# Optimization experiments

Measured on AMD Instinct MI355X. Metric: run time of the kernel, lower is better.

The kernel has to match this reference:

```python
import jax, jax.numpy as jnp
import numpy as np

EPS = 1e-8
N, IN_F, H, NRBF = 1024, 64, 32, 50
CUT_UP = 5.0  # cutoff_upper; cutoff_lower = 0 -> alpha = 5/(5-0) = 1


def setup_inputs() -> dict:
    key = jax.random.key(0)
    ks = jax.random.split(key, 6)
    start = float(np.exp(-CUT_UP))  # exp(-cutoff_upper + cutoff_lower)
    means = jnp.linspace(start, 1.0, NRBF).astype(jnp.float32)
    betas = jnp.full((NRBF,), (2.0 / NRBF * (1.0 - start)) ** (-2), dtype=jnp.float32)
    return {
        "h": jax.random.normal(ks[0], (N, IN_F), jnp.float32),
        "x": jax.random.normal(ks[1], (N, 3), jnp.float32),
        "W_fc": jax.random.normal(ks[2], (IN_F, H), jnp.float32) / np.float32(np.sqrt(IN_F)),
        "W_edge": jax.random.normal(ks[3], (NRBF, H), jnp.float32) / np.float32(np.sqrt(NRBF)),
        "means": means,
        "betas": betas,
        "W1": jax.random.normal(ks[4], (H, H), jnp.float32) / np.float32(np.sqrt(H)),
        "b1": jnp.zeros((H,), jnp.float32),
        "W2": jax.random.normal(ks[5], (H, 1), jnp.float32) / np.float32(np.sqrt(H)),
        "b2": jnp.zeros((1,), jnp.float32),
    }


def reference(h, x, W_fc, W_edge, means, betas, W1, b1, W2, b2):
    hp = h @ W_fc                                      # (N, H)
    delta = x[None, :, :] - x[:, None, :]              # (N, N, 3) pairwise deltas
    s = (delta ** 2).sum(-1, keepdims=True)            # (N, N, 1) squared distance
    dist = jax.nn.relu(s) + EPS                        # note: squared distance, as in source
    delta_n = delta / jnp.sqrt(jax.nn.relu(s + EPS))   # (N, N, 3)
    # ExpNormalSmearing: cosine_cutoff(dist) * exp(-betas*(exp(-dist) - means)^2)
    cut = 0.5 * (jnp.cos(jnp.pi * (2.0 * dist / CUT_UP + 1.0)) + 1.0)
    rbf = cut * jnp.exp(-betas * (jnp.exp(-dist) - means) ** 2)  # (N, N, NRBF)
    he = rbf @ W_edge                                  # (N, N, H)
    h_e_vec = he[..., :, None] * delta_n[..., None, :] # (N, N, H, 3)
    ese = hp[:, None, :] + hp[None, :, :]              # (N, N, H)
    comb = ese[..., None] * h_e_vec                    # (N, N, H, 3)
    cnorm = (comb ** 2).sum(-1)                        # (N, N, H)
    e = jax.nn.sigmoid(cnorm @ W1 + b1) @ W2 + b2      # (N, N, 1)
    return e.sum(axis=(-2, -3))                        # (1,)
```

## Files before the change

kernel.cpp:

```cpp
#include <hip/hip_runtime.h>
#include <hip/hip_bf16.h>
#include <math.h>

#define N_ATOMS 1024
#define IN_F 64
#define H_DIM 32
#define NRBF 50
#define TILE 16
#define NT 64
#define NBT 2080
#define TBL 4096
#define SASTR 40

typedef short bf16x8 __attribute__((ext_vector_type(8)));
typedef float f32x4  __attribute__((ext_vector_type(4)));

static __device__ __forceinline__ unsigned short f2bf(float f) {
    unsigned int u = __float_as_uint(f);
    u += 0x7fffu + ((u >> 16) & 1u);
    return (unsigned short)(u >> 16);
}

__global__ __launch_bounds__(256) void prep_kernel(
    const float* __restrict__ h, const float* __restrict__ W_fc,
    const float* __restrict__ W_edge, const float* __restrict__ means,
    const float* __restrict__ betas, const float* __restrict__ W1,
    const float* __restrict__ b1, const float* __restrict__ W2,
    float* __restrict__ hp, unsigned short* __restrict__ Gb,
    unsigned short* __restrict__ Wp, float2* __restrict__ bw,
    int* __restrict__ tt)
{
    const int blk = blockIdx.x;
    const int t = threadIdx.x;
    if (blk < 128) {
        int id = blk * 256 + t;
        int i = id >> 5, o = id & 31;
        float acc = 0.f;
        #pragma unroll 8
        for (int k = 0; k < IN_F; ++k)
            acc += h[i * IN_F + k] * W_fc[k * H_DIM + o];
        hp[i * H_DIM + o] = acc;
    } else if (blk < 192) {
        int id = (blk - 128) * 256 + t;
        int idx = id >> 2, c0 = (id & 3) * 8;
        float ed = (float)idx * (1.0f / (float)(TBL - 1));
        float acc[8];
        #pragma unroll
        for (int c = 0; c < 8; ++c) acc[c] = 0.f;
        for (int k = 0; k < NRBF; ++k) {
            float d = ed - means[k];
            float wv = __expf(-betas[k] * d * d);
            #pragma unroll
            for (int c = 0; c < 8; ++c)
                acc[c] += wv * W_edge[k * H_DIM + c0 + c];
        }
        bf16x8 pk;
        #pragma unroll
        for (int c = 0; c < 8; ++c) pk[c] = (short)f2bf(acc[c]);
        *(bf16x8*)&Gb[idx * H_DIM + c0] = pk;
    } else if (blk < 201) {
        int e = (blk - 192) * 256 + t;
        if (e < NBT) {
            int ti = (int)(64.5f - sqrtf(64.5f * 64.5f - 2.0f * (float)e));
            ti = ti < 0 ? 0 : (ti > NT - 1 ? NT - 1 : ti);
            while ((ti + 1) * NT - ((ti + 1) * ti) / 2 <= e) ++ti;
            while (ti > 0 && ti * NT - (ti * (ti - 1)) / 2 > e) --ti;
            int tj = ti + (e - (ti * NT - (ti * (ti - 1)) / 2));
            tt[e] = (ti << 8) | tj;
        }
    } else {
        #pragma unroll
        for (int q = 0; q < 4; ++q) {
            int f  = t * 4 + q;
            int ct = f >> 9, ln = (f >> 3) & 63, j = f & 7;
            int c0f = ln & 15, kb = (ln >> 4) * 8;
            Wp[f] = f2bf(W1[(kb + j) * H_DIM + c0f + 16 * ct]);
        }
        if (t < 32) { float2 v; v.x = b1[t]; v.y = W2[t]; bw[t] = v; }
    }
}

__global__ __launch_bounds__(256, 6) void pair_kernel(
    const float* __restrict__ x, const float* __restrict__ hp,
    const unsigned short* __restrict__ Gb, const unsigned short* __restrict__ Wp,
    const float2* __restrict__ bw, const int* __restrict__ tt,
    float* __restrict__ partials)
{
    __shared__ float shpi[TILE][36], shpj[TILE][36];
    __shared__ unsigned short sA[256 * SASTR];
    __shared__ float swave[4];

    const int t    = threadIdx.x;
    const int lane = t & 63;
    const int w    = t >> 6;
    const int c0f  = lane & 15;
    const int b    = blockIdx.x;

    const int tv = tt[b];
    const int ti = tv >> 8, tj = tv & 255;
    const int i0 = ti * TILE, j0 = tj * TILE;
    const float wgt = (ti == tj) ? 1.0f : 2.0f;

    const int li = t >> 4;
    const int lj = t & 15;

    const float xi0 = x[(i0 + li) * 3 + 0];
    const float xi1 = x[(i0 + li) * 3 + 1];
    const float xi2 = x[(i0 + li) * 3 + 2];
    const float xj0 = x[(j0 + lj) * 3 + 0];
    const float xj1 = x[(j0 + lj) * 3 + 1];
    const float xj2 = x[(j0 + lj) * 3 + 2];

    if (t < 128) {
        int r = t >> 3, c = t & 7;
        *(float4*)&shpi[r][c * 4] = *(const float4*)&hp[(i0 + r) * H_DIM + c * 4];
    } else {
        int u = t - 128, r = u >> 3, c = u & 7;
        *(float4*)&shpj[r][c * 4] = *(const float4*)&hp[(j0 + r) * H_DIM + c * 4];
    }

    bf16x8 bfrag0 = *(const bf16x8*)&Wp[lane * 8];
    bf16x8 bfrag1 = *(const bf16x8*)&Wp[512 + lane * 8];
    const float2 bw0 = bw[c0f];
    const float2 bw1 = bw[c0f + 16];

    const float dx = xj0 - xi0, dy = xj1 - xi1, dz = xj2 - xi2;
    const float s  = dx * dx + dy * dy + dz * dz;
    const float dist = s + 1e-8f;
    const float dn2  = s / (s + 1e-8f);
    const float sn   = __sinf(0.62831853f * dist);
    const float K    = dn2 * (sn * sn) * (sn * sn);
    const float ed   = __expf(-dist);

    float uu = ed * (float)(TBL - 1);
    int idx  = (int)(uu + 0.5f);
    if (idx > TBL - 1) idx = TBL - 1;
    const unsigned short* __restrict__ r0 = Gb + idx * H_DIM;
    const bf16x8 gA = *(const bf16x8*)(r0);
    const bf16x8 gB = *(const bf16x8*)(r0 + 8);
    const bf16x8 gC = *(const bf16x8*)(r0 + 16);
    const bf16x8 gD = *(const bf16x8*)(r0 + 24);

    __syncthreads();

    const int sw = (t >> 3) & 3;
    #pragma unroll
    for (int q = 0; q < 4; ++q) {
        const bf16x8 gs = (q == 0) ? gA : (q == 1) ? gB : (q == 2) ? gC : gD;
        union { bf16x8 v8; unsigned int u[4]; } gu, pk;
        gu.v8 = gs;
        const float4 hi0 = *(const float4*)&shpi[li][q * 8];
        const float4 hi1 = *(const float4*)&shpi[li][q * 8 + 4];
        const float4 hj0 = *(const float4*)&shpj[lj][q * 8];
        const float4 hj1 = *(const float4*)&shpj[lj][q * 8 + 4];
        float e0 = hi0.x + hj0.x, e1 = hi0.y + hj0.y;
        float e2 = hi0.z + hj0.z, e3 = hi0.w + hj0.w;
        float e4 = hi1.x + hj1.x, e5 = hi1.y + hj1.y;
        float e6 = hi1.z + hj1.z, e7 = hi1.w + hj1.w;
        float g0 = __uint_as_float(gu.u[0] << 16);
        float g1 = __uint_as_float(gu.u[0] & 0xffff0000u);
        float g2 = __uint_as_float(gu.u[1] << 16);
        float g3 = __uint_as_float(gu.u[1] & 0xffff0000u);
        float g4 = __uint_as_float(gu.u[2] << 16);
        float g5 = __uint_as_float(gu.u[2] & 0xffff0000u);
        float g6 = __uint_as_float(gu.u[3] << 16);
        float g7 = __uint_as_float(gu.u[3] & 0xffff0000u);
        float v0 = e0 * g0, v1 = e1 * g1, v2 = e2 * g2, v3 = e3 * g3;
        float v4 = e4 * g4, v5 = e5 * g5, v6 = e6 * g6, v7 = e7 * g7;
        float c0 = v0 * v0 * K, c1 = v1 * v1 * K, c2 = v2 * v2 * K, c3 = v3 * v3 * K;
        float c4 = v4 * v4 * K, c5 = v5 * v5 * K, c6 = v6 * v6 * K, c7 = v7 * v7 * K;
        pk.u[0] = ((__float_as_uint(c0) + 0x8000u) >> 16) | ((__float_as_uint(c1) + 0x8000u) & 0xffff0000u);
        pk.u[1] = ((__float_as_uint(c2) + 0x8000u) >> 16) | ((__float_as_uint(c3) + 0x8000u) & 0xffff0000u);
        pk.u[2] = ((__float_as_uint(c4) + 0x8000u) >> 16) | ((__float_as_uint(c5) + 0x8000u) & 0xffff0000u);
        pk.u[3] = ((__float_as_uint(c6) + 0x8000u) >> 16) | ((__float_as_uint(c7) + 0x8000u) & 0xffff0000u);
        *(bf16x8*)&sA[t * SASTR + (q ^ sw) * 8] = pk.v8;
    }
    __syncthreads();

    float p = 0.f;
    #pragma unroll
    for (int rt = 0; rt < 4; ++rt) {
        const int row = w * 64 + rt * 16 + c0f;
        const int rq  = (lane >> 4) ^ ((row >> 3) & 3);
        bf16x8 afrag = *(const bf16x8*)&sA[row * SASTR + rq * 8];
        f32x4 acc0 = {0.f, 0.f, 0.f, 0.f};
        acc0 = __builtin_amdgcn_mfma_f32_16x16x32_bf16(afrag, bfrag0, acc0, 0, 0, 0);
        f32x4 acc1 = {0.f, 0.f, 0.f, 0.f};
        acc1 = __builtin_amdgcn_mfma_f32_16x16x32_bf16(afrag, bfrag1, acc1, 0, 0, 0);
        #pragma unroll
        for (int r = 0; r < 4; ++r) {
            const float av0 = acc0[r] + bw0.x;
            p += bw0.y * __builtin_amdgcn_rcpf(1.0f + __expf(-av0));
            const float av1 = acc1[r] + bw1.x;
            p += bw1.y * __builtin_amdgcn_rcpf(1.0f + __expf(-av1));
        }
    }

    float v = wgt * p;
    #pragma unroll
    for (int off = 32; off > 0; off >>= 1)
        v += __shfl_down(v, off);
    if (lane == 0) swave[w] = v;
    __syncthreads();
    if (t == 0)
        partials[b] = (swave[0] + swave[1]) + (swave[2] + swave[3]);
}

__global__ __launch_bounds__(256) void reduce_kernel(
    const float* __restrict__ partials, const float* __restrict__ b2,
    float* __restrict__ out)
{
    __shared__ float sm[256];
    const int t = threadIdx.x;
    float a = 0.f;
    for (int u = t; u < NBT; u += 256) a += partials[u];
    sm[t] = a;
    __syncthreads();
    for (int off = 128; off > 0; off >>= 1) {
        if (t < off) sm[t] += sm[t + off];
        __syncthreads();
    }
    if (t == 0)
        out[0] = sm[0] + (float)N_ATOMS * (float)N_ATOMS * b2[0];
}

extern "C" void kernel_launch(void* const* d_in, const int* in_sizes, int n_in,
                              void* d_out, int out_size, void* d_ws, size_t ws_size,
                              hipStream_t stream) {
    const float* h      = (const float*)d_in[0];
    const float* x      = (const float*)d_in[1];
    const float* W_fc   = (const float*)d_in[2];
    const float* W_edge = (const float*)d_in[3];
    const float* means  = (const float*)d_in[4];
    const float* betas  = (const float*)d_in[5];
    const float* W1     = (const float*)d_in[6];
    const float* b1     = (const float*)d_in[7];
    const float* W2     = (const float*)d_in[8];
    const float* b2     = (const float*)d_in[9];
    float* out = (float*)d_out;

    char* base = (char*)d_ws;
    float*          ws_partials = (float*)base;
    float*          ws_hp       = (float*)(base + 10240);
    unsigned short* ws_Gb       = (unsigned short*)(base + 141312);
    unsigned short* ws_Wp       = (unsigned short*)(base + 403456);
    float2*         ws_bw       = (float2*)(base + 405504);
    int*            ws_tt       = (int*)(base + 405760);

    prep_kernel<<<202, 256, 0, stream>>>(h, W_fc, W_edge, means, betas,
                                         W1, b1, W2, ws_hp, ws_Gb, ws_Wp,
                                         ws_bw, ws_tt);
    pair_kernel<<<NBT, 256, 0, stream>>>(x, ws_hp, ws_Gb, ws_Wp, ws_bw,
                                         ws_tt, ws_partials);
    reduce_kernel<<<1, 256, 0, stream>>>(ws_partials, b2, out);
}
```

Before: 24.22 us.

## Build MFMA A-fragments directly in registers, dropping LDS staging and syncs

Each lane now computes the pair features for exactly the MFMA A-fragment slot it owns (row i, column j, k-slice), so the LDS staging buffer, the hp tiles in shared memory and two barriers go away. The RBF lookup table is stored as fp32 instead of bf16, so each lane fetches two float4s for its k-slice. The pair geometry (distance, sine, exp) is now recomputed by every k-slice lane, four times more often than before, and hp and x are read straight from global or cache. Occupancy is raised to 8 blocks per SM through the launch bounds.

```diff
diff --git a/kernel.cpp b/kernel.cpp
--- a/kernel.cpp
+++ b/kernel.cpp
@@ -10,7 +10,6 @@
 #define NT 64
 #define NBT 2080
 #define TBL 4096
-#define SASTR 40
 
 typedef short bf16x8 __attribute__((ext_vector_type(8)));
 typedef float f32x4  __attribute__((ext_vector_type(4)));
@@ -26,7 +25,7 @@
     const float* __restrict__ W_edge, const float* __restrict__ means,
     const float* __restrict__ betas, const float* __restrict__ W1,
     const float* __restrict__ b1, const float* __restrict__ W2,
-    float* __restrict__ hp, unsigned short* __restrict__ Gb,
+    float* __restrict__ hp, float* __restrict__ Gf,
     unsigned short* __restrict__ Wp, float2* __restrict__ bw,
     int* __restrict__ tt)
 {
@@ -54,10 +53,8 @@
             for (int c = 0; c < 8; ++c)
                 acc[c] += wv * W_edge[k * H_DIM + c0 + c];
         }
-        bf16x8 pk;
-        #pragma unroll
-        for (int c = 0; c < 8; ++c) pk[c] = (short)f2bf(acc[c]);
-        *(bf16x8*)&Gb[idx * H_DIM + c0] = pk;
+        #pragma unroll
+        for (int c = 0; c < 8; ++c) Gf[idx * H_DIM + c0 + c] = acc[c];
     } else if (blk < 201) {
         int e = (blk - 192) * 256 + t;
         if (e < NBT) {
@@ -80,20 +77,19 @@
     }
 }
 
-__global__ __launch_bounds__(256, 6) void pair_kernel(
+__global__ __launch_bounds__(256, 8) void pair_kernel(
     const float* __restrict__ x, const float* __restrict__ hp,
-    const unsigned short* __restrict__ Gb, const unsigned short* __restrict__ Wp,
+    const float* __restrict__ Gf, const unsigned short* __restrict__ Wp,
     const float2* __restrict__ bw, const int* __restrict__ tt,
     float* __restrict__ partials)
 {
-    __shared__ float shpi[TILE][36], shpj[TILE][36];
-    __shared__ unsigned short sA[256 * SASTR];
     __shared__ float swave[4];
 
     const int t    = threadIdx.x;
     const int lane = t & 63;
     const int w    = t >> 6;
     const int c0f  = lane & 15;
+    const int kb   = (lane >> 4) * 8;
     const int b    = blockIdx.x;
 
     const int tv = tt[b];
@@ -101,92 +97,69 @@
     const int i0 = ti * TILE, j0 = tj * TILE;
     const float wgt = (ti == tj) ? 1.0f : 2.0f;
 
-    const int li = t >> 4;
-    const int lj = t & 15;
-
-    const float xi0 = x[(i0 + li) * 3 + 0];
-    const float xi1 = x[(i0 + li) * 3 + 1];
-    const float xi2 = x[(i0 + li) * 3 + 2];
-    const float xj0 = x[(j0 + lj) * 3 + 0];
-    const float xj1 = x[(j0 + lj) * 3 + 1];
-    const float xj2 = x[(j0 + lj) * 3 + 2];
-
-    if (t < 128) {
-        int r = t >> 3, c = t & 7;
-        *(float4*)&shpi[r][c * 4] = *(const float4*)&hp[(i0 + r) * H_DIM + c * 4];
-    } else {
-        int u = t - 128, r = u >> 3, c = u & 7;
-        *(float4*)&shpj[r][c * 4] = *(const float4*)&hp[(j0 + r) * H_DIM + c * 4];
-    }
-
-    bf16x8 bfrag0 = *(const bf16x8*)&Wp[lane * 8];
-    bf16x8 bfrag1 = *(const bf16x8*)&Wp[512 + lane * 8];
+    const float4 hja = *(const float4*)&hp[(j0 + c0f) * H_DIM + kb];
+    const float4 hjb = *(const float4*)&hp[(j0 + c0f) * H_DIM + kb + 4];
+    const float xj0 = x[(j0 + c0f) * 3 + 0];
+    const float xj1 = x[(j0 + c0f) * 3 + 1];
+    const float xj2 = x[(j0 + c0f) * 3 + 2];
+
+    const bf16x8 bfrag0 = *(const bf16x8*)&Wp[lane * 8];
+    const bf16x8 bfrag1 = *(const bf16x8*)&Wp[512 + lane * 8];
     const float2 bw0 = bw[c0f];
     const float2 bw1 = bw[c0f + 16];
 
-    const float dx = xj0 - xi0, dy = xj1 - xi1, dz = xj2 - xi2;
-    const float s  = dx * dx + dy * dy + dz * dz;
-    const float dist = s + 1e-8f;
-    const float dn2  = s / (s + 1e-8f);
-    const float sn   = __sinf(0.62831853f * dist);
-    const float K    = dn2 * (sn * sn) * (sn * sn);
-    const float ed   = __expf(-dist);
-
-    float uu = ed * (float)(TBL - 1);
-    int idx  = (int)(uu + 0.5f);
-    if (idx > TBL - 1) idx = TBL - 1;
-    const unsigned short* __restrict__ r0 = Gb + idx * H_DIM;
-    const bf16x8 gA = *(const bf16x8*)(r0);
-    const bf16x8 gB = *(const bf16x8*)(r0 + 8);
-    const bf16x8 gC = *(const bf16x8*)(r0 + 16);
-    const bf16x8 gD = *(const bf16x8*)(r0 + 24);
-
-    __syncthreads();
-
-    const int sw = (t >> 3) & 3;
+    float p = 0.f;
+
     #pragma unroll
-    for (int q = 0; q < 4; ++q) {
-        const bf16x8 gs = (q == 0) ? gA : (q == 1) ? gB : (q == 2) ? gC : gD;
-        union { bf16x8 v8; unsigned int u[4]; } gu, pk;
-        gu.v8 = gs;
-        const float4 hi0 = *(const float4*)&shpi[li][q * 8];
-        const float4 hi1 = *(const float4*)&shpi[li][q * 8 + 4];
-        const float4 hj0 = *(const float4*)&shpj[lj][q * 8];
-        const float4 hj1 = *(const float4*)&shpj[lj][q * 8 + 4];
-        float e0 = hi0.x + hj0.x, e1 = hi0.y + hj0.y;
-        float e2 = hi0.z + hj0.z, e3 = hi0.w + hj0.w;
-        float e4 = hi1.x + hj1.x, e5 = hi1.y + hj1.y;
-        float e6 = hi1.z + hj1.z, e7 = hi1.w + hj1.w;
-        float g0 = __uint_as_float(gu.u[0] << 16);
-        float g1 = __uint_as_float(gu.u[0] & 0xffff0000u);
-        float g2 = __uint_as_float(gu.u[1] << 16);
-        float g3 = __uint_as_float(gu.u[1] & 0xffff0000u);
-        float g4 = __uint_as_float(gu.u[2] << 16);
-        float g5 = __uint_as_float(gu.u[2] & 0xffff0000u);
-        float g6 = __uint_as_float(gu.u[3] << 16);
-        float g7 = __uint_as_float(gu.u[3] & 0xffff0000u);
-        float v0 = e0 * g0, v1 = e1 * g1, v2 = e2 * g2, v3 = e3 * g3;
-        float v4 = e4 * g4, v5 = e5 * g5, v6 = e6 * g6, v7 = e7 * g7;
-        float c0 = v0 * v0 * K, c1 = v1 * v1 * K, c2 = v2 * v2 * K, c3 = v3 * v3 * K;
-        float c4 = v4 * v4 * K, c5 = v5 * v5 * K, c6 = v6 * v6 * K, c7 = v7 * v7 * K;
+    for (int rt = 0; rt < 4; ++rt) {
+        const int ri = w * 4 + rt;
+        const float xi0 = x[(i0 + ri) * 3 + 0];
+        const float xi1 = x[(i0 + ri) * 3 + 1];
+        const float xi2 = x[(i0 + ri) * 3 + 2];
+
+        const float dx = xj0 - xi0, dy = xj1 - xi1, dz = xj2 - xi2;
+        const float s  = dx * dx + dy * dy + dz * dz;
+        const float dist = s + 1e-8f;
+        const float dn2  = s / (s + 1e-8f);
+        const float sn   = __sinf(0.62831853f * dist);
+        const float K    = dn2 * (sn * sn) * (sn * sn);
+        const float ed   = __expf(-dist);
+
+        float uu = ed * (float)(TBL - 1);
+        int idx  = (int)(uu + 0.5f);
+        if (idx > TBL - 1) idx = TBL - 1;
+
+        const float* __restrict__ gp = Gf + idx * H_DIM + kb;
+        const float4 ga = *(const float4*)gp;
+        const float4 gb = *(const float4*)(gp + 4);
+
+        const float4 hia = *(const float4*)&hp[(i0 + ri) * H_DIM + kb];
+        const float4 hib = *(const float4*)&hp[(i0 + ri) * H_DIM + kb + 4];
+
+        const float v0 = (hia.x + hja.x) * ga.x;
+        const float v1 = (hia.y + hja.y) * ga.y;
+        const float v2 = (hia.z + hja.z) * ga.z;
+        const float v3 = (hia.w + hja.w) * ga.w;
+        const float v4 = (hib.x + hjb.x) * gb.x;
+        const float v5 = (hib.y + hjb.y) * gb.y;
+        const float v6 = (hib.z + hjb.z) * gb.z;
+        const float v7 = (hib.w + hjb.w) * gb.w;
+        const float c0 = v0 * v0 * K, c1 = v1 * v1 * K;
+        const float c2 = v2 * v2 * K, c3 = v3 * v3 * K;
+        const float c4 = v4 * v4 * K, c5 = v5 * v5 * K;
+        const float c6 = v6 * v6 * K, c7 = v7 * v7 * K;
+
+        union { bf16x8 v8; unsigned int u[4]; } pk;
         pk.u[0] = ((__float_as_uint(c0) + 0x8000u) >> 16) | ((__float_as_uint(c1) + 0x8000u) & 0xffff0000u);
         pk.u[1] = ((__float_as_uint(c2) + 0x8000u) >> 16) | ((__float_as_uint(c3) + 0x8000u) & 0xffff0000u);
         pk.u[2] = ((__float_as_uint(c4) + 0x8000u) >> 16) | ((__float_as_uint(c5) + 0x8000u) & 0xffff0000u);
         pk.u[3] = ((__float_as_uint(c6) + 0x8000u) >> 16) | ((__float_as_uint(c7) + 0x8000u) & 0xffff0000u);
-        *(bf16x8*)&sA[t * SASTR + (q ^ sw) * 8] = pk.v8;
-    }
-    __syncthreads();
-
-    float p = 0.f;
-    #pragma unroll
-    for (int rt = 0; rt < 4; ++rt) {
-        const int row = w * 64 + rt * 16 + c0f;
-        const int rq  = (lane >> 4) ^ ((row >> 3) & 3);
-        bf16x8 afrag = *(const bf16x8*)&sA[row * SASTR + rq * 8];
+
         f32x4 acc0 = {0.f, 0.f, 0.f, 0.f};
-        acc0 = __builtin_amdgcn_mfma_f32_16x16x32_bf16(afrag, bfrag0, acc0, 0, 0, 0);
+        acc0 = __builtin_amdgcn_mfma_f32_16x16x32_bf16(pk.v8, bfrag0, acc0, 0, 0, 0);
         f32x4 acc1 = {0.f, 0.f, 0.f, 0.f};
-        acc1 = __builtin_amdgcn_mfma_f32_16x16x32_bf16(afrag, bfrag1, acc1, 0, 0, 0);
+        acc1 = __builtin_amdgcn_mfma_f32_16x16x32_bf16(pk.v8, bfrag1, acc1, 0, 0, 0);
+
         #pragma unroll
         for (int r = 0; r < 4; ++r) {
             const float av0 = acc0[r] + bw0.x;
@@ -242,15 +215,15 @@
     char* base = (char*)d_ws;
     float*          ws_partials = (float*)base;
     float*          ws_hp       = (float*)(base + 10240);
-    unsigned short* ws_Gb       = (unsigned short*)(base + 141312);
-    unsigned short* ws_Wp       = (unsigned short*)(base + 403456);
-    float2*         ws_bw       = (float2*)(base + 405504);
-    int*            ws_tt       = (int*)(base + 405760);
+    float*          ws_Gf       = (float*)(base + 141312);
+    unsigned short* ws_Wp       = (unsigned short*)(base + 665600);
+    float2*         ws_bw       = (float2*)(base + 667648);
+    int*            ws_tt       = (int*)(base + 667904);
 
     prep_kernel<<<202, 256, 0, stream>>>(h, W_fc, W_edge, means, betas,
-                                         W1, b1, W2, ws_hp, ws_Gb, ws_Wp,
+                                         W1, b1, W2, ws_hp, ws_Gf, ws_Wp,
                                          ws_bw, ws_tt);
-    pair_kernel<<<NBT, 256, 0, stream>>>(x, ws_hp, ws_Gb, ws_Wp, ws_bw,
+    pair_kernel<<<NBT, 256, 0, stream>>>(x, ws_hp, ws_Gf, ws_Wp, ws_bw,
                                          ws_tt, ws_partials);
     reduce_kernel<<<1, 256, 0, stream>>>(ws_partials, b2, out);
 }
```

Result: slower. 34.50 us (+42.4%).

## Process two j-tiles per block to halve block count in pair kernel

Applied to the files above, without the earlier changes.

Each block now handles one 16-row i-tile against a 32-column j-strip split into two 16x16 sub-tiles, with the triangular tile enumeration remapped to row pairs. This halves the number of blocks and reuses the i-side positions and hp rows across both sub-tiles, cutting per-block setup and launch overhead. The lower-triangle sub-tile is skipped through a zero weight. The change adds an extra barrier, serialises the two sub-tiles within a block, raises register pressure, and lowers the occupancy hint from 6 to 5.

```diff
diff --git a/kernel.cpp b/kernel.cpp
--- a/kernel.cpp
+++ b/kernel.cpp
@@ -8,7 +8,7 @@
 #define NRBF 50
 #define TILE 16
 #define NT 64
-#define NBT 2080
+#define NBLK 1056
 #define TBL 4096
 #define SASTR 40
 
@@ -58,15 +58,18 @@
         #pragma unroll
         for (int c = 0; c < 8; ++c) pk[c] = (short)f2bf(acc[c]);
         *(bf16x8*)&Gb[idx * H_DIM + c0] = pk;
-    } else if (blk < 201) {
+    } else if (blk < 197) {
         int e = (blk - 192) * 256 + t;
-        if (e < NBT) {
-            int ti = (int)(64.5f - sqrtf(64.5f * 64.5f - 2.0f * (float)e));
-            ti = ti < 0 ? 0 : (ti > NT - 1 ? NT - 1 : ti);
-            while ((ti + 1) * NT - ((ti + 1) * ti) / 2 <= e) ++ti;
-            while (ti > 0 && ti * NT - (ti * (ti - 1)) / 2 > e) --ti;
-            int tj = ti + (e - (ti * NT - (ti * (ti - 1)) / 2));
-            tt[e] = (ti << 8) | tj;
+        if (e < NBLK) {
+            int a = (int)((65.0f - sqrtf(65.0f * 65.0f - 4.0f * (float)e)) * 0.5f);
+            a = a < 0 ? 0 : (a > 31 ? 31 : a);
+            while (a > 0 && a * (65 - a) > e) --a;
+            while ((a + 1) * (65 - (a + 1)) <= e) ++a;
+            int e1 = e - a * (65 - a);
+            int ti, tj2;
+            if (e1 < 32 - a) { ti = 2 * a;     tj2 = a + e1; }
+            else             { ti = 2 * a + 1; tj2 = a + e1 - (32 - a); }
+            tt[e] = (ti << 8) | tj2;
         }
     } else {
         #pragma unroll
@@ -80,13 +83,13 @@
     }
 }
 
-__global__ __launch_bounds__(256, 6) void pair_kernel(
+__global__ __launch_bounds__(256, 5) void pair_kernel(
     const float* __restrict__ x, const float* __restrict__ hp,
     const unsigned short* __restrict__ Gb, const unsigned short* __restrict__ Wp,
     const float2* __restrict__ bw, const int* __restrict__ tt,
     float* __restrict__ partials)
 {
-    __shared__ float shpi[TILE][36], shpj[TILE][36];
+    __shared__ float shpi[TILE][36], shpjA[TILE][36], shpjB[TILE][36];
     __shared__ unsigned short sA[256 * SASTR];
     __shared__ float swave[4];
 
@@ -96,10 +99,13 @@
     const int c0f  = lane & 15;
     const int b    = blockIdx.x;
 
-    const int tv = tt[b];
-    const int ti = tv >> 8, tj = tv & 255;
-    const int i0 = ti * TILE, j0 = tj * TILE;
-    const float wgt = (ti == tj) ? 1.0f : 2.0f;
+    const int tv  = tt[b];
+    const int ti  = tv >> 8, tj2 = tv & 255;
+    const int i0  = ti * TILE;
+    const int j0A = tj2 * 32, j0B = j0A + 16;
+    const int tjA = 2 * tj2, tjB = tjA + 1;
+    const float wgtA = (tjA < ti) ? 0.f : (tjA == ti ? 1.f : 2.f);
+    const float wgtB = (tjB == ti) ? 1.f : 2.f;
 
     const int li = t >> 4;
     const int lj = t & 15;
@@ -107,96 +113,168 @@
     const float xi0 = x[(i0 + li) * 3 + 0];
     const float xi1 = x[(i0 + li) * 3 + 1];
     const float xi2 = x[(i0 + li) * 3 + 2];
-    const float xj0 = x[(j0 + lj) * 3 + 0];
-    const float xj1 = x[(j0 + lj) * 3 + 1];
-    const float xj2 = x[(j0 + lj) * 3 + 2];
+    const float xA0 = x[(j0A + lj) * 3 + 0];
+    const float xA1 = x[(j0A + lj) * 3 + 1];
+    const float xA2 = x[(j0A + lj) * 3 + 2];
+    const float xB0 = x[(j0B + lj) * 3 + 0];
+    const float xB1 = x[(j0B + lj) * 3 + 1];
+    const float xB2 = x[(j0B + lj) * 3 + 2];
 
     if (t < 128) {
         int r = t >> 3, c = t & 7;
-        *(float4*)&shpi[r][c * 4] = *(const float4*)&hp[(i0 + r) * H_DIM + c * 4];
+        *(float4*)&shpi[r][c * 4]  = *(const float4*)&hp[(i0 + r) * H_DIM + c * 4];
+        *(float4*)&shpjB[r][c * 4] = *(const float4*)&hp[(j0B + r) * H_DIM + c * 4];
     } else {
         int u = t - 128, r = u >> 3, c = u & 7;
-        *(float4*)&shpj[r][c * 4] = *(const float4*)&hp[(j0 + r) * H_DIM + c * 4];
-    }
-
-    bf16x8 bfrag0 = *(const bf16x8*)&Wp[lane * 8];
-    bf16x8 bfrag1 = *(const bf16x8*)&Wp[512 + lane * 8];
+        *(float4*)&shpjA[r][c * 4] = *(const float4*)&hp[(j0A + r) * H_DIM + c * 4];
+    }
+
+    const bf16x8 bfrag0 = *(const bf16x8*)&Wp[lane * 8];
+    const bf16x8 bfrag1 = *(const bf16x8*)&Wp[512 + lane * 8];
     const float2 bw0 = bw[c0f];
     const float2 bw1 = bw[c0f + 16];
 
-    const float dx = xj0 - xi0, dy = xj1 - xi1, dz = xj2 - xi2;
-    const float s  = dx * dx + dy * dy + dz * dz;
-    const float dist = s + 1e-8f;
-    const float dn2  = s / (s + 1e-8f);
-    const float sn   = __sinf(0.62831853f * dist);
-    const float K    = dn2 * (sn * sn) * (sn * sn);
-    const float ed   = __expf(-dist);
-
-    float uu = ed * (float)(TBL - 1);
-    int idx  = (int)(uu + 0.5f);
-    if (idx > TBL - 1) idx = TBL - 1;
-    const unsigned short* __restrict__ r0 = Gb + idx * H_DIM;
-    const bf16x8 gA = *(const bf16x8*)(r0);
-    const bf16x8 gB = *(const bf16x8*)(r0 + 8);
-    const bf16x8 gC = *(const bf16x8*)(r0 + 16);
-    const bf16x8 gD = *(const bf16x8*)(r0 + 24);
+    float dx = xA0 - xi0, dy = xA1 - xi1, dz = xA2 - xi2;
+    float sA_ = dx * dx + dy * dy + dz * dz;
+    const float distA = sA_ + 1e-8f;
+    const float dn2A  = sA_ / (sA_ + 1e-8f);
+    const float snA   = __sinf(0.62831853f * distA);
+    const float KA    = dn2A * (snA * snA) * (snA * snA);
+    const float edA   = __expf(-distA);
+    float uuA = edA * (float)(TBL - 1);
+    int idxA  = (int)(uuA + 0.5f);
+    if (idxA > TBL - 1) idxA = TBL - 1;
+    const unsigned short* __restrict__ rA = Gb + idxA * H_DIM;
+    const bf16x8 gA0 = *(const bf16x8*)(rA);
+    const bf16x8 gA1 = *(const bf16x8*)(rA + 8);
+    const bf16x8 gA2 = *(const bf16x8*)(rA + 16);
+    const bf16x8 gA3 = *(const bf16x8*)(rA + 24);
+
+    dx = xB0 - xi0; dy = xB1 - xi1; dz = xB2 - xi2;
+    float sB_ = dx * dx + dy * dy + dz * dz;
+    const float distB = sB_ + 1e-8f;
+    const float dn2B  = sB_ / (sB_ + 1e-8f);
+    const float snB   = __sinf(0.62831853f * distB);
+    const float KB    = dn2B * (snB * snB) * (snB * snB);
+    const float edB   = __expf(-distB);
+    float uuB = edB * (float)(TBL - 1);
+    int idxB  = (int)(uuB + 0.5f);
+    if (idxB > TBL - 1) idxB = TBL - 1;
+    const unsigned short* __restrict__ rB = Gb + idxB * H_DIM;
+    const bf16x8 gB0 = *(const bf16x8*)(rB);
+    const bf16x8 gB1 = *(const bf16x8*)(rB + 8);
+    const bf16x8 gB2 = *(const bf16x8*)(rB + 16);
+    const bf16x8 gB3 = *(const bf16x8*)(rB + 24);
 
     __syncthreads();
 
     const int sw = (t >> 3) & 3;
-    #pragma unroll
-    for (int q = 0; q < 4; ++q) {
-        const bf16x8 gs = (q == 0) ? gA : (q == 1) ? gB : (q == 2) ? gC : gD;
-        union { bf16x8 v8; unsigned int u[4]; } gu, pk;
-        gu.v8 = gs;
-        const float4 hi0 = *(const float4*)&shpi[li][q * 8];
-        const float4 hi1 = *(const float4*)&shpi[li][q * 8 + 4];
-        const float4 hj0 = *(const float4*)&shpj[lj][q * 8];
-        const float4 hj1 = *(const float4*)&shpj[lj][q * 8 + 4];
-        float e0 = hi0.x + hj0.x, e1 = hi0.y + hj0.y;
-        float e2 = hi0.z + hj0.z, e3 = hi0.w + hj0.w;
-        float e4 = hi1.x + hj1.x, e5 = hi1.y + hj1.y;
-        float e6 = hi1.z + hj1.z, e7 = hi1.w + hj1.w;
-        float g0 = __uint_as_float(gu.u[0] << 16);
-        float g1 = __uint_as_float(gu.u[0] & 0xffff0000u);
-        float g2 = __uint_as_float(gu.u[1] << 16);
-        float g3 = __uint_as_float(gu.u[1] & 0xffff0000u);
-        float g4 = __uint_as_float(gu.u[2] << 16);
-        float g5 = __uint_as_float(gu.u[2] & 0xffff0000u);
-        float g6 = __uint_as_float(gu.u[3] << 16);
-        float g7 = __uint_as_float(gu.u[3] & 0xffff0000u);
-        float v0 = e0 * g0, v1 = e1 * g1, v2 = e2 * g2, v3 = e3 * g3;
-        float v4 = e4 * g4, v5 = e5 * g5, v6 = e6 * g6, v7 = e7 * g7;
-        float c0 = v0 * v0 * K, c1 = v1 * v1 * K, c2 = v2 * v2 * K, c3 = v3 * v3 * K;
-        float c4 = v4 * v4 * K, c5 = v5 * v5 * K, c6 = v6 * v6 * K, c7 = v7 * v7 * K;
-        pk.u[0] = ((__float_as_uint(c0) + 0x8000u) >> 16) | ((__float_as_uint(c1) + 0x8000u) & 0xffff0000u);
-        pk.u[1] = ((__float_as_uint(c2) + 0x8000u) >> 16) | ((__float_as_uint(c3) + 0x8000u) & 0xffff0000u);
-        pk.u[2] = ((__float_as_uint(c4) + 0x8000u) >> 16) | ((__float_as_uint(c5) + 0x8000u) & 0xffff0000u);
-        pk.u[3] = ((__float_as_uint(c6) + 0x8000u) >> 16) | ((__float_as_uint(c7) + 0x8000u) & 0xffff0000u);
-        *(bf16x8*)&sA[t * SASTR + (q ^ sw) * 8] = pk.v8;
-    }
-    __syncthreads();
-
     float p = 0.f;
-    #pragma unroll
-    for (int rt = 0; rt < 4; ++rt) {
-        const int row = w * 64 + rt * 16 + c0f;
-        const int rq  = (lane >> 4) ^ ((row >> 3) & 3);
-        bf16x8 afrag = *(const bf16x8*)&sA[row * SASTR + rq * 8];
-        f32x4 acc0 = {0.f, 0.f, 0.f, 0.f};
-        acc0 = __builtin_amdgcn_mfma_f32_16x16x32_bf16(afrag, bfrag0, acc0, 0, 0, 0);
-        f32x4 acc1 = {0.f, 0.f, 0.f, 0.f};
-        acc1 = __builtin_amdgcn_mfma_f32_16x16x32_bf16(afrag, bfrag1, acc1, 0, 0, 0);
-        #pragma unroll
-        for (int r = 0; r < 4; ++r) {
-            const float av0 = acc0[r] + bw0.x;
-            p += bw0.y * __builtin_amdgcn_rcpf(1.0f + __expf(-av0));
-            const float av1 = acc1[r] + bw1.x;
-            p += bw1.y * __builtin_amdgcn_rcpf(1.0f + __expf(-av1));
-        }
-    }
-
-    float v = wgt * p;
+
+    if (wgtA != 0.f) {
+        #pragma unroll
+        for (int q = 0; q < 4; ++q) {
+            const bf16x8 gs = (q == 0) ? gA0 : (q == 1) ? gA1 : (q == 2) ? gA2 : gA3;
+            union { bf16x8 v8; unsigned int u[4]; } gu, pk;
+            gu.v8 = gs;
+            const float4 hi0 = *(const float4*)&shpi[li][q * 8];
+            const float4 hi1 = *(const float4*)&shpi[li][q * 8 + 4];
+            const float4 hj0 = *(const float4*)&shpjA[lj][q * 8];
+            const float4 hj1 = *(const float4*)&shpjA[lj][q * 8 + 4];
+            float g0 = __uint_as_float(gu.u[0] << 16);
+            float g1 = __uint_as_float(gu.u[0] & 0xffff0000u);
+            float g2 = __uint_as_float(gu.u[1] << 16);
+            float g3 = __uint_as_float(gu.u[1] & 0xffff0000u);
+            float g4 = __uint_as_float(gu.u[2] << 16);
+            float g5 = __uint_as_float(gu.u[2] & 0xffff0000u);
+            float g6 = __uint_as_float(gu.u[3] << 16);
+            float g7 = __uint_as_float(gu.u[3] & 0xffff0000u);
+            float v0 = (hi0.x + hj0.x) * g0, v1 = (hi0.y + hj0.y) * g1;
+            float v2 = (hi0.z + hj0.z) * g2, v3 = (hi0.w + hj0.w) * g3;
+            float v4 = (hi1.x + hj1.x) * g4, v5 = (hi1.y + hj1.y) * g5;
+            float v6 = (hi1.z + hj1.z) * g6, v7 = (hi1.w + hj1.w) * g7;
+            float c0 = v0 * v0 * KA, c1 = v1 * v1 * KA, c2 = v2 * v2 * KA, c3 = v3 * v3 * KA;
+            float c4 = v4 * v4 * KA, c5 = v5 * v5 * KA, c6 = v6 * v6 * KA, c7 = v7 * v7 * KA;
+            pk.u[0] = ((__float_as_uint(c0) + 0x8000u) >> 16) | ((__float_as_uint(c1) + 0x8000u) & 0xffff0000u);
+            pk.u[1] = ((__float_as_uint(c2) + 0x8000u) >> 16) | ((__float_as_uint(c3) + 0x8000u) & 0xffff0000u);
+            pk.u[2] = ((__float_as_uint(c4) + 0x8000u) >> 16) | ((__float_as_uint(c5) + 0x8000u) & 0xffff0000u);
+            pk.u[3] = ((__float_as_uint(c6) + 0x8000u) >> 16) | ((__float_as_uint(c7) + 0x8000u) & 0xffff0000u);
+            *(bf16x8*)&sA[t * SASTR + (q ^ sw) * 8] = pk.v8;
+        }
+        __syncthreads();
+
+        float pA = 0.f;
+        #pragma unroll
+        for (int rt = 0; rt < 4; ++rt) {
+            const int row = w * 64 + rt * 16 + c0f;
+            const int rq  = (lane >> 4) ^ ((row >> 3) & 3);
+            bf16x8 afrag = *(const bf16x8*)&sA[row * SASTR + rq * 8];
+            f32x4 acc0 = {0.f, 0.f, 0.f, 0.f};
+            acc0 = __builtin_amdgcn_mfma_f32_16x16x32_bf16(afrag, bfrag0, acc0, 0, 0, 0);
+            f32x4 acc1 = {0.f, 0.f, 0.f, 0.f};
+            acc1 = __builtin_amdgcn_mfma_f32_16x16x32_bf16(afrag, bfrag1, acc1, 0, 0, 0);
+            #pragma unroll
+            for (int r = 0; r < 4; ++r) {
+                pA += bw0.y * __builtin_amdgcn_rcpf(1.0f + __expf(-(acc0[r] + bw0.x)));
+                pA += bw1.y * __builtin_amdgcn_rcpf(1.0f + __expf(-(acc1[r] + bw1.x)));
+            }
+        }
+        p += wgtA * pA;
+        __syncthreads();
+    }
+
+    {
+        #pragma unroll
+        for (int q = 0; q < 4; ++q) {
+            const bf16x8 gs = (q == 0) ? gB0 : (q == 1) ? gB1 : (q == 2) ? gB2 : gB3;
+            union { bf16x8 v8; unsigned int u[4]; } gu, pk;
+            gu.v8 = gs;
+            const float4 hi0 = *(const float4*)&shpi[li][q * 8];
+            const float4 hi1 = *(const float4*)&shpi[li][q * 8 + 4];
+            const float4 hj0 = *(const float4*)&shpjB[lj][q * 8];
+            const float4 hj1 = *(const float4*)&shpjB[lj][q * 8 + 4];
+            float g0 = __uint_as_float(gu.u[0] << 16);
+            float g1 = __uint_as_float(gu.u[0] & 0xffff0000u);
+            float g2 = __uint_as_float(gu.u[1] << 16);
+            float g3 = __uint_as_float(gu.u[1] & 0xffff0000u);
+            float g4 = __uint_as_float(gu.u[2] << 16);
+            float g5 = __uint_as_float(gu.u[2] & 0xffff0000u);
+            float g6 = __uint_as_float(gu.u[3] << 16);
+            float g7 = __uint_as_float(gu.u[3] & 0xffff0000u);
+            float v0 = (hi0.x + hj0.x) * g0, v1 = (hi0.y + hj0.y) * g1;
+            float v2 = (hi0.z + hj0.z) * g2, v3 = (hi0.w + hj0.w) * g3;
+            float v4 = (hi1.x + hj1.x) * g4, v5 = (hi1.y + hj1.y) * g5;
+            float v6 = (hi1.z + hj1.z) * g6, v7 = (hi1.w + hj1.w) * g7;
+            float c0 = v0 * v0 * KB, c1 = v1 * v1 * KB, c2 = v2 * v2 * KB, c3 = v3 * v3 * KB;
+            float c4 = v4 * v4 * KB, c5 = v5 * v5 * KB, c6 = v6 * v6 * KB, c7 = v7 * v7 * KB;
+            pk.u[0] = ((__float_as_uint(c0) + 0x8000u) >> 16) | ((__float_as_uint(c1) + 0x8000u) & 0xffff0000u);
+            pk.u[1] = ((__float_as_uint(c2) + 0x8000u) >> 16) | ((__float_as_uint(c3) + 0x8000u) & 0xffff0000u);
+            pk.u[2] = ((__float_as_uint(c4) + 0x8000u) >> 16) | ((__float_as_uint(c5) + 0x8000u) & 0xffff0000u);
+            pk.u[3] = ((__float_as_uint(c6) + 0x8000u) >> 16) | ((__float_as_uint(c7) + 0x8000u) & 0xffff0000u);
+            *(bf16x8*)&sA[t * SASTR + (q ^ sw) * 8] = pk.v8;
+        }
+        __syncthreads();
+
+        float pB = 0.f;
+        #pragma unroll
+        for (int rt = 0; rt < 4; ++rt) {
+            const int row = w * 64 + rt * 16 + c0f;
+            const int rq  = (lane >> 4) ^ ((row >> 3) & 3);
+            bf16x8 afrag = *(const bf16x8*)&sA[row * SASTR + rq * 8];
+            f32x4 acc0 = {0.f, 0.f, 0.f, 0.f};
+            acc0 = __builtin_amdgcn_mfma_f32_16x16x32_bf16(afrag, bfrag0, acc0, 0, 0, 0);
+            f32x4 acc1 = {0.f, 0.f, 0.f, 0.f};
+            acc1 = __builtin_amdgcn_mfma_f32_16x16x32_bf16(afrag, bfrag1, acc1, 0, 0, 0);
+            #pragma unroll
+            for (int r = 0; r < 4; ++r) {
+                pB += bw0.y * __builtin_amdgcn_rcpf(1.0f + __expf(-(acc0[r] + bw0.x)));
+                pB += bw1.y * __builtin_amdgcn_rcpf(1.0f + __expf(-(acc1[r] + bw1.x)));
+            }
+        }
+        p += wgtB * pB;
+    }
+
+    float v = p;
     #pragma unroll
     for (int off = 32; off > 0; off >>= 1)
         v += __shfl_down(v, off);
@@ -213,7 +291,7 @@
     __shared__ float sm[256];
     const int t = threadIdx.x;
     float a = 0.f;
-    for (int u = t; u < NBT; u += 256) a += partials[u];
+    for (int u = t; u < NBLK; u += 256) a += partials[u];
     sm[t] = a;
     __syncthreads();
     for (int off = 128; off > 0; off >>= 1) {
@@ -247,10 +325,10 @@
     float2*         ws_bw       = (float2*)(base + 405504);
     int*            ws_tt       = (int*)(base + 405760);
 
-    prep_kernel<<<202, 256, 0, stream>>>(h, W_fc, W_edge, means, betas,
+    prep_kernel<<<198, 256, 0, stream>>>(h, W_fc, W_edge, means, betas,
                                          W1, b1, W2, ws_hp, ws_Gb, ws_Wp,
                                          ws_bw, ws_tt);
-    pair_kernel<<<NBT, 256, 0, stream>>>(x, ws_hp, ws_Gb, ws_Wp, ws_bw,
-                                         ws_tt, ws_partials);
+    pair_kernel<<<NBLK, 256, 0, stream>>>(x, ws_hp, ws_Gb, ws_Wp, ws_bw,
+                                          ws_tt, ws_partials);
     reduce_kernel<<<1, 256, 0, stream>>>(ws_partials, b2, out);
 }
```

Result: no change. 24.64 us (+1.7%).

## Fuse final reduction into pair kernel via last-block atomic counter; window RBF table build

Applied to the files above, without the earlier changes.

Removes the separate reduce kernel launch. Each pair block publishes its partial with a release store and bumps an atomic counter, and the block that finishes last sums all partials and writes the output. The prep table build also loops only over the ~19 RBF centers near each table entry, assuming evenly spaced means and a single shared beta, and uses vector loads for W_edge. This saves a kernel launch and tail latency, at the cost of an atomic per block and extra shared memory, and the windowed table build assumes uniform means and betas.

```diff
diff --git a/kernel.cpp b/kernel.cpp
--- a/kernel.cpp
+++ b/kernel.cpp
@@ -28,7 +28,7 @@
     const float* __restrict__ b1, const float* __restrict__ W2,
     float* __restrict__ hp, unsigned short* __restrict__ Gb,
     unsigned short* __restrict__ Wp, float2* __restrict__ bw,
-    int* __restrict__ tt)
+    int* __restrict__ tt, int* __restrict__ cnt)
 {
     const int blk = blockIdx.x;
     const int t = threadIdx.x;
@@ -43,16 +43,26 @@
     } else if (blk < 192) {
         int id = (blk - 128) * 256 + t;
         int idx = id >> 2, c0 = (id & 3) * 8;
+        const float m0   = means[0];
+        const float dm   = means[1] - means[0];
+        const float beta = betas[0];
         float ed = (float)idx * (1.0f / (float)(TBL - 1));
+        int kc = (int)((ed - m0) / dm + 0.5f);
+        kc = kc < 0 ? 0 : (kc > NRBF - 1 ? NRBF - 1 : kc);
+        int k0 = kc - 9 < 0 ? 0 : kc - 9;
+        int k1 = kc + 9 > NRBF - 1 ? NRBF - 1 : kc + 9;
         float acc[8];
         #pragma unroll
         for (int c = 0; c < 8; ++c) acc[c] = 0.f;
-        for (int k = 0; k < NRBF; ++k) {
-            float d = ed - means[k];
-            float wv = __expf(-betas[k] * d * d);
-            #pragma unroll
-            for (int c = 0; c < 8; ++c)
-                acc[c] += wv * W_edge[k * H_DIM + c0 + c];
+        for (int k = k0; k <= k1; ++k) {
+            float d = ed - (m0 + (float)k * dm);
+            float wv = __expf(-beta * d * d);
+            const float4 wa = *(const float4*)&W_edge[k * H_DIM + c0];
+            const float4 wb = *(const float4*)&W_edge[k * H_DIM + c0 + 4];
+            acc[0] += wv * wa.x; acc[1] += wv * wa.y;
+            acc[2] += wv * wa.z; acc[3] += wv * wa.w;
+            acc[4] += wv * wb.x; acc[5] += wv * wb.y;
+            acc[6] += wv * wb.z; acc[7] += wv * wb.w;
         }
         bf16x8 pk;
         #pragma unroll
@@ -77,6 +87,7 @@
             Wp[f] = f2bf(W1[(kb + j) * H_DIM + c0f + 16 * ct]);
         }
         if (t < 32) { float2 v; v.x = b1[t]; v.y = W2[t]; bw[t] = v; }
+        if (t == 0) *cnt = 0;
     }
 }
 
@@ -84,11 +95,14 @@
     const float* __restrict__ x, const float* __restrict__ hp,
     const unsigned short* __restrict__ Gb, const unsigned short* __restrict__ Wp,
     const float2* __restrict__ bw, const int* __restrict__ tt,
-    float* __restrict__ partials)
+    const float* __restrict__ b2, float* __restrict__ partials,
+    int* __restrict__ cnt, float* __restrict__ out)
 {
     __shared__ float shpi[TILE][36], shpj[TILE][36];
     __shared__ unsigned short sA[256 * SASTR];
     __shared__ float swave[4];
+    __shared__ float sm[256];
+    __shared__ int isLast;
 
     const int t    = threadIdx.x;
     const int lane = t & 63;
@@ -119,8 +133,8 @@
         *(float4*)&shpj[r][c * 4] = *(const float4*)&hp[(j0 + r) * H_DIM + c * 4];
     }
 
-    bf16x8 bfrag0 = *(const bf16x8*)&Wp[lane * 8];
-    bf16x8 bfrag1 = *(const bf16x8*)&Wp[512 + lane * 8];
+    const bf16x8 bfrag0 = *(const bf16x8*)&Wp[lane * 8];
+    const bf16x8 bfrag1 = *(const bf16x8*)&Wp[512 + lane * 8];
     const float2 bw0 = bw[c0f];
     const float2 bw1 = bw[c0f + 16];
 
@@ -189,10 +203,8 @@
         acc1 = __builtin_amdgcn_mfma_f32_16x16x32_bf16(afrag, bfrag1, acc1, 0, 0, 0);
         #pragma unroll
         for (int r = 0; r < 4; ++r) {
-            const float av0 = acc0[r] + bw0.x;
-            p += bw0.y * __builtin_amdgcn_rcpf(1.0f + __expf(-av0));
-            const float av1 = acc1[r] + bw1.x;
-            p += bw1.y * __builtin_amdgcn_rcpf(1.0f + __expf(-av1));
+            p += bw0.y * __builtin_amdgcn_rcpf(1.0f + __expf(-(acc0[r] + bw0.x)));
+            p += bw1.y * __builtin_amdgcn_rcpf(1.0f + __expf(-(acc1[r] + bw1.x)));
         }
     }
 
@@ -202,26 +214,30 @@
         v += __shfl_down(v, off);
     if (lane == 0) swave[w] = v;
     __syncthreads();
-    if (t == 0)
-        partials[b] = (swave[0] + swave[1]) + (swave[2] + swave[3]);
-}
-
-__global__ __launch_bounds__(256) void reduce_kernel(
-    const float* __restrict__ partials, const float* __restrict__ b2,
-    float* __restrict__ out)
-{
-    __shared__ float sm[256];
-    const int t = threadIdx.x;
-    float a = 0.f;
-    for (int u = t; u < NBT; u += 256) a += partials[u];
-    sm[t] = a;
-    __syncthreads();
-    for (int off = 128; off > 0; off >>= 1) {
-        if (t < off) sm[t] += sm[t + off];
+    if (t == 0) {
+        float part = (swave[0] + swave[1]) + (swave[2] + swave[3]);
+        __hip_atomic_store(&partials[b], part, __ATOMIC_RELEASE,
+                           __HIP_MEMORY_SCOPE_AGENT);
+        int old = __hip_atomic_fetch_add(cnt, 1, __ATOMIC_ACQ_REL,
+                                         __HIP_MEMORY_SCOPE_AGENT);
+        isLast = (old == NBT - 1) ? 1 : 0;
+    }
+    __syncthreads();
+
+    if (isLast) {
+        float a = 0.f;
+        for (int u = t; u < NBT; u += 256)
+            a += __hip_atomic_load(&partials[u], __ATOMIC_RELAXED,
+                                   __HIP_MEMORY_SCOPE_AGENT);
+        sm[t] = a;
         __syncthreads();
-    }
-    if (t == 0)
-        out[0] = sm[0] + (float)N_ATOMS * (float)N_ATOMS * b2[0];
+        for (int off = 128; off > 0; off >>= 1) {
+            if (t < off) sm[t] += sm[t + off];
+            __syncthreads();
+        }
+        if (t == 0)
+            out[0] = sm[0] + (float)N_ATOMS * (float)N_ATOMS * b2[0];
+    }
 }
 
 extern "C" void kernel_launch(void* const* d_in, const int* in_sizes, int n_in,
@@ -246,11 +262,11 @@
     unsigned short* ws_Wp       = (unsigned short*)(base + 403456);
     float2*         ws_bw       = (float2*)(base + 405504);
     int*            ws_tt       = (int*)(base + 405760);
+    int*            ws_cnt      = (int*)(base + 414208);
 
     prep_kernel<<<202, 256, 0, stream>>>(h, W_fc, W_edge, means, betas,
                                          W1, b1, W2, ws_hp, ws_Gb, ws_Wp,
-                                         ws_bw, ws_tt);
+                                         ws_bw, ws_tt, ws_cnt);
     pair_kernel<<<NBT, 256, 0, stream>>>(x, ws_hp, ws_Gb, ws_Wp, ws_bw,
-                                         ws_tt, ws_partials);
-    reduce_kernel<<<1, 256, 0, stream>>>(ws_partials, b2, out);
-}
+                                         ws_tt, b2, ws_partials, ws_cnt, out);
+}
```

After: 68.77 us. 184% more time.
